# Kernel tuning notes

Measured on AMD Instinct MI355X. Metric: run time of the kernel, lower is better.

The kernel has to match this reference:

```python
import jax, jax.numpy as jnp
import numpy as np

SEQ, BATCH, N_IN, N_HID, N_CLS = 128, 16384, 28, 100, 10


def setup_inputs() -> dict:
    key = jax.random.key(0)
    ks = jax.random.split(key, 7)
    s_in = 1.0 / np.sqrt(N_IN)
    s_h = 1.0 / np.sqrt(N_HID)
    return {
        "data": jax.random.normal(ks[0], (SEQ, BATCH, N_IN), dtype=jnp.float32),
        "w_xh": jax.random.uniform(ks[1], (N_IN, N_HID), jnp.float32, -s_in, s_in),
        "b_xh": jax.random.uniform(ks[2], (N_HID,), jnp.float32, -s_in, s_in),
        "w_hh": jax.random.uniform(ks[3], (N_HID, N_HID), jnp.float32, -s_h, s_h),
        "b_hh": jax.random.uniform(ks[4], (N_HID,), jnp.float32, -s_h, s_h),
        "w_fc": jax.random.uniform(ks[5], (N_HID, N_CLS), jnp.float32, -s_h, s_h),
        "b_fc": jax.random.uniform(ks[6], (N_CLS,), jnp.float32, -s_h, s_h),
    }


def reference(data, w_xh, b_xh, w_hh, b_hh, w_fc, b_fc):
    # Precompute input projections for all timesteps in one big GEMM:
    # [T, B, n_in] @ [n_in, H] -> [T, B, H]
    xh = jnp.einsum("tbi,ih->tbh", data, w_xh) + b_xh + b_hh

    def step(h, xh_t):
        h = jnp.tanh(xh_t + h @ w_hh)
        return h, None

    h0 = jnp.zeros((data.shape[1], w_hh.shape[0]), dtype=data.dtype)
    h_T, _ = jax.lax.scan(step, h0, xh)
    return h_T @ w_fc + b_fc  # [B, cls]
```

## Files before the change

kernel.cpp:

```cpp
#include <hip/hip_runtime.h>


#define SEQ   128
#define BATCH 16384
#define NIN   28
#define NHID  100
#define NCLS  10

#define HSTR  136
#define WROWS 112

typedef __bf16 bf16x8 __attribute__((ext_vector_type(8)));
typedef float  f32x4  __attribute__((ext_vector_type(4)));

__device__ __forceinline__ unsigned short f2bf(float f) {
    unsigned u = __builtin_bit_cast(unsigned, f);
    u += 0x7FFFu + ((u >> 16) & 1u);
    return (unsigned short)(u >> 16);
}
__device__ __forceinline__ float bf2f(unsigned short b) {
    unsigned u = ((unsigned)b) << 16;
    return __builtin_bit_cast(float, u);
}
__device__ __forceinline__ float tanh_fast(float x) {
    float t = __expf(2.0f * x);
    float r = __builtin_amdgcn_rcpf(t + 1.0f);
    return __builtin_fmaf(-2.0f, r, 1.0f);
}
__device__ __forceinline__ unsigned cvt_pk_bf16(float lo, float hi) {
    unsigned d;
    asm("v_cvt_pk_bf16_f32 %0, %1, %2" : "=v"(d) : "v"(lo), "v"(hi));
    return d;
}

__global__ __launch_bounds__(512, 8) void rnn_fused_kernel(
    const float* __restrict__ data, const float* __restrict__ w_xh,
    const float* __restrict__ b_xh, const float* __restrict__ w_hh,
    const float* __restrict__ b_hh, const float* __restrict__ w_fc,
    const float* __restrict__ b_fc, float* __restrict__ out)
{
    __shared__ unsigned short pool[WROWS * HSTR];
    unsigned short* WT = pool;
    unsigned short* hb = pool;

    const int tid  = threadIdx.x;
    const int wid  = tid >> 6;
    const int lane = tid & 63;
    const int x    = lane & 15;
    const int g    = lane >> 4;
    const int m0   = blockIdx.x * 16;

    const bool compute = (wid < 7);

    for (int idx = tid; idx < WROWS * HSTR; idx += 512) {
        int j = idx % WROWS;
        int k = idx / WROWS;
        float v = 0.0f;
        if (j < NHID) {
            if (k < NHID)            v = w_hh[k * NHID + j];
            else if (k < NHID + NIN) v = w_xh[(k - NHID) * NHID + j];
        }
        WT[j * HSTR + k] = f2bf(v);
    }
    __syncthreads();

    bf16x8 aw[4];
    f32x4  biasf = {0.f, 0.f, 0.f, 0.f};
    if (compute) {
        #pragma unroll
        for (int kt = 0; kt < 4; ++kt)
            aw[kt] = *(const bf16x8*)&WT[(wid * 16 + x) * HSTR + kt * 32 + g * 8];
        #pragma unroll
        for (int r = 0; r < 4; ++r) {
            int j  = wid * 16 + g * 4 + r;
            int jc = (j < NHID) ? j : (NHID - 1);
            biasf[r] = b_xh[jc] + b_hh[jc];
        }
    }
    __syncthreads();

    {
        unsigned int* hb32 = (unsigned int*)hb;
        for (int idx = tid; idx < (16 * HSTR) / 2; idx += 512) hb32[idx] = 0u;
    }
    __syncthreads();
    if (tid < 224) {
        float2 v = *(const float2*)(data + (size_t)m0 * NIN + 2 * tid);
        int m = tid / 14, i2 = 2 * (tid - m * 14);
        *(unsigned int*)&hb[m * HSTR + NHID + i2] = cvt_pk_bf16(v.x, v.y);
    }
    __syncthreads();

    for (int t = 0; t < SEQ; ++t) {
        unsigned short* cur = hb + (t & 1) * (16 * HSTR);
        unsigned short* nxt = hb + ((t & 1) ^ 1) * (16 * HSTR);

        if (compute) {
            bf16x8 bq[4];
            #pragma unroll
            for (int kt = 0; kt < 4; ++kt)
                bq[kt] = *(const bf16x8*)&cur[x * HSTR + kt * 32 + g * 8];

            f32x4 acc = biasf;
            #pragma unroll
            for (int kt = 0; kt < 4; ++kt)
                acc = __builtin_amdgcn_mfma_f32_16x16x32_bf16(aw[kt], bq[kt], acc, 0, 0, 0);

            float t0 = tanh_fast(acc[0]);
            float t1 = tanh_fast(acc[1]);
            float t2 = tanh_fast(acc[2]);
            float t3 = tanh_fast(acc[3]);
            int j0 = wid * 16 + 4 * g;
            if (j0 < NHID) {
                unsigned lo = cvt_pk_bf16(t0, t1);
                unsigned hi = cvt_pk_bf16(t2, t3);
                unsigned long long q = ((unsigned long long)hi << 32) | (unsigned long long)lo;
                *(unsigned long long*)&nxt[x * HSTR + j0] = q;
            }
        } else {
            int t1s = (t < SEQ - 1) ? t + 1 : t;
            const float* src = data + ((size_t)t1s * BATCH + m0) * NIN;
            float2 xv[4];
            #pragma unroll
            for (int r = 0; r < 4; ++r) {
                int idx = r * 64 + lane;
                if (idx < 224) xv[r] = *(const float2*)(src + 2 * idx);
            }
            #pragma unroll
            for (int r = 0; r < 4; ++r) {
                int idx = r * 64 + lane;
                if (idx < 224) {
                    int m = idx / 14, i2 = 2 * (idx - m * 14);
                    *(unsigned int*)&nxt[m * HSTR + NHID + i2] = cvt_pk_bf16(xv[r].x, xv[r].y);
                }
            }
        }
        __syncthreads();
    }

    for (int o = tid; o < 16 * NCLS; o += 512) {
        int m = o / NCLS, c = o - (o / NCLS) * NCLS;
        float s = b_fc[c];
        for (int j = 0; j < NHID; ++j)
            s = __builtin_fmaf(bf2f(hb[m * HSTR + j]), w_fc[j * NCLS + c], s);
        out[(size_t)(m0 + m) * NCLS + c] = s;
    }
}

extern "C" void kernel_launch(void* const* d_in, const int* in_sizes, int n_in,
                              void* d_out, int out_size, void* d_ws, size_t ws_size,
                              hipStream_t stream) {
    const float* data = (const float*)d_in[0];
    const float* w_xh = (const float*)d_in[1];
    const float* b_xh = (const float*)d_in[2];
    const float* w_hh = (const float*)d_in[3];
    const float* b_hh = (const float*)d_in[4];
    const float* w_fc = (const float*)d_in[5];
    const float* b_fc = (const float*)d_in[6];
    float* outp = (float*)d_out;
    (void)in_sizes; (void)n_in; (void)out_size; (void)d_ws; (void)ws_size;
    rnn_fused_kernel<<<dim3(BATCH / 16), dim3(512), 0, stream>>>(
        data, w_xh, b_xh, w_hh, b_hh, w_fc, b_fc, outp);
}
```

Measured before the change: 376.8 us.

## Retile RNN recurrence: 32 rows per block, 4 waves each owning multiple hidden tiles

Each block now handles 32 batch rows with 256 threads, and the kernel launches half as many blocks. Each wave covers one 16-row M tile and either 4 or 3 hidden-column tiles, keeping those W slices in registers, instead of one wave per column tile plus a dedicated loader wave. Input loading moves into the compute waves with jg==1 and is prefetched two timesteps ahead in registers. This cuts barrier participants and loader idle time per step and raises MFMA work per wave. The costs are more registers, fewer resident waves per CU, and imbalanced work between the two wave groups, since the jg==1 waves do 3 tiles plus loads.

```diff
diff --git a/kernel.cpp b/kernel.cpp
--- a/kernel.cpp
+++ b/kernel.cpp
@@ -9,6 +9,7 @@
 
 #define HSTR  136
 #define WROWS 112
+#define RPB   32
 
 typedef __bf16 bf16x8 __attribute__((ext_vector_type(8)));
 typedef float  f32x4  __attribute__((ext_vector_type(4)));
@@ -33,7 +34,7 @@
     return d;
 }
 
-__global__ __launch_bounds__(512, 8) void rnn_fused_kernel(
+__global__ __launch_bounds__(256, 2) void rnn_fused_kernel(
     const float* __restrict__ data, const float* __restrict__ w_xh,
     const float* __restrict__ b_xh, const float* __restrict__ w_hh,
     const float* __restrict__ b_hh, const float* __restrict__ w_fc,
@@ -48,11 +49,15 @@
     const int lane = tid & 63;
     const int x    = lane & 15;
     const int g    = lane >> 4;
-    const int m0   = blockIdx.x * 16;
+    const int jg   = wid & 1;
+    const int mt   = wid >> 1;
+    const int bm0  = blockIdx.x * RPB;
 
-    const bool compute = (wid < 7);
+    const int NJT    = jg ? 3 : 4;
+    const int JTBASE = jg ? 4 : 0;
+    const int row    = mt * 16 + x;
 
-    for (int idx = tid; idx < WROWS * HSTR; idx += 512) {
+    for (int idx = tid; idx < WROWS * HSTR; idx += 256) {
         int j = idx % WROWS;
         int k = idx / WROWS;
         float v = 0.0f;
@@ -64,86 +69,114 @@
     }
     __syncthreads();
 
-    bf16x8 aw[4];
-    f32x4  biasf = {0.f, 0.f, 0.f, 0.f};
-    if (compute) {
-        #pragma unroll
-        for (int kt = 0; kt < 4; ++kt)
-            aw[kt] = *(const bf16x8*)&WT[(wid * 16 + x) * HSTR + kt * 32 + g * 8];
-        #pragma unroll
-        for (int r = 0; r < 4; ++r) {
-            int j  = wid * 16 + g * 4 + r;
-            int jc = (j < NHID) ? j : (NHID - 1);
-            biasf[r] = b_xh[jc] + b_hh[jc];
+    bf16x8 aw[4][4];
+    f32x4  biasf[4];
+    #pragma unroll
+    for (int n = 0; n < 4; ++n) {
+        if (n < NJT) {
+            int jt = JTBASE + n;
+            #pragma unroll
+            for (int kt = 0; kt < 4; ++kt)
+                aw[n][kt] = *(const bf16x8*)&WT[(jt * 16 + x) * HSTR + kt * 32 + g * 8];
+            #pragma unroll
+            for (int r = 0; r < 4; ++r) {
+                int j  = jt * 16 + g * 4 + r;
+                int jc = (j < NHID) ? j : (NHID - 1);
+                biasf[n][r] = b_xh[jc] + b_hh[jc];
+            }
         }
     }
     __syncthreads();
 
     {
         unsigned int* hb32 = (unsigned int*)hb;
-        for (int idx = tid; idx < (16 * HSTR) / 2; idx += 512) hb32[idx] = 0u;
+        for (int idx = tid; idx < (2 * RPB * HSTR) / 2; idx += 256) hb32[idx] = 0u;
     }
     __syncthreads();
-    if (tid < 224) {
-        float2 v = *(const float2*)(data + (size_t)m0 * NIN + 2 * tid);
-        int m = tid / 14, i2 = 2 * (tid - m * 14);
-        *(unsigned int*)&hb[m * HSTR + NHID + i2] = cvt_pk_bf16(v.x, v.y);
+    #pragma unroll
+    for (int r = 0; r < 2; ++r) {
+        int idx = r * 256 + tid;
+        if (idx < RPB * 14) {
+            float2 v = *(const float2*)(data + (size_t)bm0 * NIN + 2 * idx);
+            int m = idx / 14, i2 = 2 * (idx - m * 14);
+            *(unsigned int*)&hb[m * HSTR + NHID + i2] = cvt_pk_bf16(v.x, v.y);
+        }
+    }
+    float2 xv[4];
+    if (jg == 1) {
+        const float* src = data + ((size_t)1 * BATCH + bm0 + mt * 16) * NIN;
+        #pragma unroll
+        for (int r = 0; r < 4; ++r) {
+            int idx = r * 64 + lane;
+            if (idx < 224) xv[r] = *(const float2*)(src + 2 * idx);
+        }
     }
     __syncthreads();
 
     for (int t = 0; t < SEQ; ++t) {
-        unsigned short* cur = hb + (t & 1) * (16 * HSTR);
-        unsigned short* nxt = hb + ((t & 1) ^ 1) * (16 * HSTR);
+        unsigned short* cur = hb + (t & 1) * (RPB * HSTR);
+        unsigned short* nxt = hb + ((t & 1) ^ 1) * (RPB * HSTR);
 
-        if (compute) {
-            bf16x8 bq[4];
+        if (jg == 1) {
             #pragma unroll
-            for (int kt = 0; kt < 4; ++kt)
-                bq[kt] = *(const bf16x8*)&cur[x * HSTR + kt * 32 + g * 8];
-
-            f32x4 acc = biasf;
-            #pragma unroll
-            for (int kt = 0; kt < 4; ++kt)
-                acc = __builtin_amdgcn_mfma_f32_16x16x32_bf16(aw[kt], bq[kt], acc, 0, 0, 0);
-
-            float t0 = tanh_fast(acc[0]);
-            float t1 = tanh_fast(acc[1]);
-            float t2 = tanh_fast(acc[2]);
-            float t3 = tanh_fast(acc[3]);
-            int j0 = wid * 16 + 4 * g;
-            if (j0 < NHID) {
-                unsigned lo = cvt_pk_bf16(t0, t1);
-                unsigned hi = cvt_pk_bf16(t2, t3);
-                unsigned long long q = ((unsigned long long)hi << 32) | (unsigned long long)lo;
-                *(unsigned long long*)&nxt[x * HSTR + j0] = q;
+            for (int r = 0; r < 4; ++r) {
+                int idx = r * 64 + lane;
+                if (idx < 224) {
+                    int m = idx / 14, i2 = 2 * (idx - m * 14);
+                    *(unsigned int*)&nxt[(mt * 16 + m) * HSTR + NHID + i2] =
+                        cvt_pk_bf16(xv[r].x, xv[r].y);
+                }
             }
-        } else {
-            int t1s = (t < SEQ - 1) ? t + 1 : t;
-            const float* src = data + ((size_t)t1s * BATCH + m0) * NIN;
-            float2 xv[4];
+            int tL = (t + 2 < SEQ) ? t + 2 : SEQ - 1;
+            const float* src = data + ((size_t)tL * BATCH + bm0 + mt * 16) * NIN;
             #pragma unroll
             for (int r = 0; r < 4; ++r) {
                 int idx = r * 64 + lane;
                 if (idx < 224) xv[r] = *(const float2*)(src + 2 * idx);
             }
+        }
+
+        bf16x8 bq[4];
+        #pragma unroll
+        for (int kt = 0; kt < 4; ++kt)
+            bq[kt] = *(const bf16x8*)&cur[row * HSTR + kt * 32 + g * 8];
+
+        f32x4 acc[4];
+        #pragma unroll
+        for (int n = 0; n < 4; ++n)
+            if (n < NJT) acc[n] = biasf[n];
+        #pragma unroll
+        for (int kt = 0; kt < 4; ++kt)
             #pragma unroll
-            for (int r = 0; r < 4; ++r) {
-                int idx = r * 64 + lane;
-                if (idx < 224) {
-                    int m = idx / 14, i2 = 2 * (idx - m * 14);
-                    *(unsigned int*)&nxt[m * HSTR + NHID + i2] = cvt_pk_bf16(xv[r].x, xv[r].y);
+            for (int n = 0; n < 4; ++n)
+                if (n < NJT)
+                    acc[n] = __builtin_amdgcn_mfma_f32_16x16x32_bf16(aw[n][kt], bq[kt], acc[n], 0, 0, 0);
+
+        #pragma unroll
+        for (int n = 0; n < 4; ++n) {
+            if (n < NJT) {
+                int j0 = (JTBASE + n) * 16 + 4 * g;
+                float t0 = tanh_fast(acc[n][0]);
+                float t1 = tanh_fast(acc[n][1]);
+                float t2 = tanh_fast(acc[n][2]);
+                float t3 = tanh_fast(acc[n][3]);
+                if (j0 < NHID) {
+                    unsigned lo = cvt_pk_bf16(t0, t1);
+                    unsigned hi = cvt_pk_bf16(t2, t3);
+                    unsigned long long q = ((unsigned long long)hi << 32) | (unsigned long long)lo;
+                    *(unsigned long long*)&nxt[row * HSTR + j0] = q;
                 }
             }
         }
         __syncthreads();
     }
 
-    for (int o = tid; o < 16 * NCLS; o += 512) {
+    for (int o = tid; o < RPB * NCLS; o += 256) {
         int m = o / NCLS, c = o - (o / NCLS) * NCLS;
         float s = b_fc[c];
         for (int j = 0; j < NHID; ++j)
             s = __builtin_fmaf(bf2f(hb[m * HSTR + j]), w_fc[j * NCLS + c], s);
-        out[(size_t)(m0 + m) * NCLS + c] = s;
+        out[(size_t)(bm0 + m) * NCLS + c] = s;
     }
 }
 
@@ -159,6 +192,6 @@
     const float* b_fc = (const float*)d_in[6];
     float* outp = (float*)d_out;
     (void)in_sizes; (void)n_in; (void)out_size; (void)d_ws; (void)ws_size;
-    rnn_fused_kernel<<<dim3(BATCH / 16), dim3(512), 0, stream>>>(
+    rnn_fused_kernel<<<dim3(BATCH / RPB), dim3(256), 0, stream>>>(
         data, w_xh, b_xh, w_hh, b_hh, w_fc, b_fc, outp);
 }
```

New measurement: 382.4 us. Within noise of the previous version (+1.5%).
